# Optimization experiments

Measured on AMD Instinct MI355X. Metric: run time of the kernel, lower is better.

## Reference

```python
import jax, jax.numpy as jnp
import numpy as np

EPS = 1e-5
OFFSET_SCALE = 1.0
KPTS = 9   # 3x3 deformable kernel
GROUP = 1  # in_dim // out_dim


def _bn(x, g, b, m, v):
    # eval-mode BatchNorm2d on (B,C,H,W)
    s = g / jnp.sqrt(v + EPS)
    return x * s[None, :, None, None] + (b - m * s)[None, :, None, None]


def _dcnv4_core(value, offset, mask, offset_scale):
    # value: (B,H,W,G,Cg); offset: (B,H,W,G,K,2) as (dx,dy); mask: (B,H,W,G,K)
    B, H, W, G, Cg = value.shape
    K = mask.shape[-1]
    dt = value.dtype
    ky = jnp.repeat(jnp.arange(3) - 1, 3).astype(dt)
    kx = jnp.tile(jnp.arange(3) - 1, 3).astype(dt)
    grid = jnp.stack([kx, ky], -1)                                   # (K,2)
    base = jnp.stack(jnp.meshgrid(jnp.arange(W, dtype=dt),
                                  jnp.arange(H, dtype=dt),
                                  indexing='xy'), -1)                # (H,W,2) = (x,y)
    loc = base[None, :, :, None, None, :] + (grid + offset) * offset_scale  # (B,H,W,G,K,2)
    px, py = loc[..., 0], loc[..., 1]
    x0 = jnp.floor(px); y0 = jnp.floor(py)
    fx = px - x0; fy = py - y0
    vflat = value.transpose(0, 3, 1, 2, 4).reshape(B, G, H * W, Cg)
    out = jnp.zeros((B, G, H * W, Cg), dt)
    corners = ((0.0, 0.0, (1 - fx) * (1 - fy)), (1.0, 0.0, fx * (1 - fy)),
               (0.0, 1.0, (1 - fx) * fy), (1.0, 1.0, fx * fy))
    for dx, dy, wgt in corners:
        xi = x0 + dx; yi = y0 + dy
        valid = ((xi >= 0) & (xi < W) & (yi >= 0) & (yi < H)).astype(dt)
        idx = (jnp.clip(yi, 0, W and H - 1) * W + jnp.clip(xi, 0, W - 1)).astype(jnp.int32)
        idx = idx.transpose(0, 3, 1, 2, 4).reshape(B, G, H * W * K)
        v = jnp.take_along_axis(vflat, idx[..., None], axis=2).reshape(B, G, H * W, K, Cg)
        w = (wgt * valid * mask).transpose(0, 3, 1, 2, 4).reshape(B, G, H * W, K)
        out = out + jnp.einsum('bgsk,bgskc->bgsc', w, v)
    return out.reshape(B, G, H, W, Cg).transpose(0, 2, 3, 1, 4).reshape(B, H, W, G * Cg)


def setup_inputs() -> dict:
    key = jax.random.key(0)
    B, C, H, W = 8, 128, 64, 64
    C_OUT = 128
    OM = ((GROUP * KPTS * 3 + 7) // 8) * 8  # 32, offset_mask padded width
    ks = jax.random.split(key, 16)
    f = jnp.float32
    sc = 1.0 / np.sqrt(C).astype(np.float32)
    return {
        'x': jax.random.normal(ks[0], (B, C, H, W), f),
        'bn1_g': jax.random.uniform(ks[1], (C,), f, 0.5, 1.5),
        'bn1_b': jax.random.normal(ks[2], (C,), f) * 0.1,
        'bn1_m': jax.random.normal(ks[3], (C,), f) * 0.1,
        'bn1_v': jax.random.uniform(ks[4], (C,), f, 0.5, 1.5),
        'w_pw0': jax.random.normal(ks[5], (C, C), f) * sc,
        'w_vp': jax.random.normal(ks[6], (C, C), f) * sc,
        'b_vp': jnp.zeros((C,), f),
        'w_om': jax.random.normal(ks[7], (C, OM), f) * 0.01,
        'b_om': jnp.zeros((OM,), f),
        'w_op': jax.random.normal(ks[8], (C, C), f) * sc,
        'bn2_g': jax.random.uniform(ks[9], (C,), f, 0.5, 1.5),
        'bn2_b': jax.random.normal(ks[10], (C,), f) * 0.1,
        'bn2_m': jax.random.normal(ks[11], (C,), f) * 0.1,
        'bn2_v': jax.random.uniform(ks[12], (C,), f, 0.5, 1.5),
        'w_pw1': jax.random.normal(ks[13], (C_OUT, C), f) * sc,
    }


def reference(x, bn1_g, bn1_b, bn1_m, bn1_v, w_pw0, w_vp, b_vp, w_om, b_om, w_op,
              bn2_g, bn2_b, bn2_m, bn2_v, w_pw1):
    x = _bn(x, bn1_g, bn1_b, bn1_m, bn1_v)
    x = jnp.einsum('bchw,oc->bohw', x, w_pw0)
    B, C, H, W = x.shape
    x = x.reshape(B, H * W, C)  # raw reshape (faithful to torch .reshape, NOT a permute)
    G, K = GROUP, KPTS
    Cg = C // G
    value = (x @ w_vp + b_vp).reshape(B, H, W, G, Cg)
    om = (x @ w_om + b_om)[..., :G * K * 3].reshape(B, H, W, G, K, 3)
    out = _dcnv4_core(value, om[..., :2], om[..., 2], OFFSET_SCALE)
    out = out.reshape(B, H * W, C) @ w_op
    x = out.reshape(B, C, H, W)  # raw reshape back
    x = _bn(x, bn2_g, bn2_b, bn2_m, bn2_v)
    x = jnp.einsum('bchw,oc->bohw', x, w_pw1)
    return x
```

## Files before the change

### kernel.cpp

```cpp
#include <hip/hip_runtime.h>

#define HW 4096
#define PADF 33
#define PADU 136
typedef unsigned short ushort;
typedef __attribute__((ext_vector_type(8))) short short8;
typedef __attribute__((ext_vector_type(4))) float f32x4;

__device__ __forceinline__ ushort bf_rne(float f) {
  unsigned u = __float_as_uint(f);
  unsigned r = (u + 0x7fffu + ((u >> 16) & 1u)) >> 16;
  return (ushort)r;
}
__device__ __forceinline__ void split2(float f, ushort& hi, ushort& lo) {
  ushort h = bf_rne(f);
  float hf = __uint_as_float((unsigned)h << 16);
  hi = h;
  lo = bf_rne(f - hf);
}

__global__ __launch_bounds__(256) void prep(
    const float* __restrict__ g1, const float* __restrict__ be1,
    const float* __restrict__ m1, const float* __restrict__ v1,
    const float* __restrict__ w0,
    const float* __restrict__ g2, const float* __restrict__ be2,
    const float* __restrict__ m2, const float* __restrict__ v2,
    const float* __restrict__ w1,
    const float* __restrict__ wvp, const float* __restrict__ wom,
    const float* __restrict__ wop,
    ushort* __restrict__ W0h, ushort* __restrict__ W0l, float* __restrict__ b0,
    ushort* __restrict__ W1h, ushort* __restrict__ W1l, float* __restrict__ b1,
    ushort* __restrict__ vph, ushort* __restrict__ vpl,
    ushort* __restrict__ oph, ushort* __restrict__ opl,
    ushort* __restrict__ omh, ushort* __restrict__ oml)
{
  const int t = threadIdx.x;
  const int role = blockIdx.x;
  if (role < 16) {
    __shared__ float sc[128], sh[128], part[16][17];
    const int cv = role >> 3;
    const float* g  = cv ? g2 : g1;
    const float* be = cv ? be2 : be1;
    const float* mm = cv ? m2 : m1;
    const float* vv = cv ? v2 : v1;
    if (t < 128) {
      float s = g[t] / sqrtf(vv[t] + 1e-5f);
      sc[t] = s;
      sh[t] = be[t] - mm[t] * s;
    }
    __syncthreads();
    const float* ws = cv ? w1 : w0;
    ushort* dh = cv ? W1h : W0h;
    ushort* dl = cv ? W1l : W0l;
    float* bb  = cv ? b1 : b0;
    const int o = ((role & 7) << 4) + (t >> 4);
    const int kl = t & 15;
    float accb = 0.f;
    #pragma unroll
    for (int j = 0; j < 8; ++j) {
      const int k = (kl << 3) + j;
      const float wv = ws[o * 128 + k];
      ushort hi, lo;
      split2(wv * sc[k], hi, lo);
      dh[o * 128 + k] = hi;
      dl[o * 128 + k] = lo;
      accb = fmaf(wv, sh[k], accb);
    }
    part[t >> 4][kl] = accb;
    __syncthreads();
    if (kl == 0) {
      float s = 0.f;
      #pragma unroll
      for (int j = 0; j < 16; ++j) s += part[t >> 4][j];
      bb[o] = s;
    }
  } else if (role < 32) {
    const int rr = role & 7;
    const float* srcM = (role < 24) ? wvp : wop;
    ushort* dh = (role < 24) ? vph : oph;
    ushort* dl = (role < 24) ? vpl : opl;
    const int n = (rr << 4) + (t >> 4);
    const int kl = t & 15;
    #pragma unroll
    for (int j = 0; j < 8; ++j) {
      const int k = (kl << 3) + j;
      ushort hi, lo;
      split2(srcM[k * 128 + n], hi, lo);
      dh[n * 128 + k] = hi;
      dl[n * 128 + k] = lo;
    }
  } else {
    const int n = ((role - 32) << 4) + (t >> 4);
    const int kl = t & 15;
    #pragma unroll
    for (int j = 0; j < 8; ++j) {
      const int k = (kl << 3) + j;
      ushort hi, lo;
      split2(wom[k * 32 + n], hi, lo);
      omh[n * 128 + k] = hi;
      oml[n * 128 + k] = lo;
    }
  }
}

__global__ __launch_bounds__(512, 2) void fused_x_valom(
    const float* __restrict__ x,
    const ushort* __restrict__ W0h, const ushort* __restrict__ W0l,
    const float* __restrict__ b0,
    const ushort* __restrict__ vph, const ushort* __restrict__ vpl,
    const float* __restrict__ bvp, const float* __restrict__ bom,
    float* __restrict__ value, float* __restrict__ omb)
{
  __shared__ __align__(16) char smem[102912];
  __shared__ float b0_s[128], b2_s[160];
  ushort (*Wh_s)[32] = (ushort(*)[32])(smem);
  ushort (*Wl_s)[32] = (ushort(*)[32])(smem + 8192);
  float*  Xf         = (float*)(smem + 16384);
  ushort (*Vh_s)[32] = (ushort(*)[32])(smem);
  ushort (*Vl_s)[32] = (ushort(*)[32])(smem + 10240);
  ushort (*Yh)[PADU] = (ushort(*)[PADU])(smem + 33280);
  ushort (*Yl)[PADU] = (ushort(*)[PADU])(smem + 68096);

  const int t = threadIdx.x;
  const int cb = blockIdx.x;
  const int b = blockIdx.y;
  const int hwBase = cb << 7;
  const size_t xbase = (size_t)b * (size_t)(128 * HW);
  if (t < 128) b0_s[t] = b0[t];
  if (t < 160) b2_s[t] = (t < 128) ? bvp[t] : bom[t - 128];
  const int lane = t & 63, w = t >> 6;
  const int col = lane & 15, quad = lane >> 4;
  const f32x4 z = {0.f, 0.f, 0.f, 0.f};

  f32x4 acc1[8];
  #pragma unroll
  for (int f = 0; f < 8; ++f) acc1[f] = z;

  for (int kc = 0; kc < 4; ++kc) {
    const int kB = kc << 5;
    {
      const int o = t >> 2, q8 = (t & 3) << 3;
      *(uint4*)&Wh_s[o][q8] = *(const uint4*)&W0h[o * 128 + kB + q8];
      *(uint4*)&Wl_s[o][q8] = *(const uint4*)&W0l[o * 128 + kB + q8];
    }
    #pragma unroll
    for (int p = 0; p < 2; ++p) {
      const int idx = (p << 9) + t;
      const int c = idx >> 5, j4 = (idx & 31) << 2;
      const float4 f = *(const float4*)&x[xbase + (size_t)(kB + c) * HW + hwBase + j4];
      Xf[(j4 + 0) * PADF + c] = f.x;
      Xf[(j4 + 1) * PADF + c] = f.y;
      Xf[(j4 + 2) * PADF + c] = f.z;
      Xf[(j4 + 3) * PADF + c] = f.w;
    }
    __syncthreads();
    union { ushort u[8]; short8 v; } bh, bl;
    {
      const float* xr = &Xf[((w << 4) + col) * PADF + (quad << 3)];
      #pragma unroll
      for (int j = 0; j < 8; ++j) split2(xr[j], bh.u[j], bl.u[j]);
    }
    #pragma unroll
    for (int f = 0; f < 8; ++f) {
      const int row = (f << 4) + col;
      const short8 aH = *(const short8*)&Wh_s[row][quad << 3];
      const short8 aL = *(const short8*)&Wl_s[row][quad << 3];
      acc1[f] = __builtin_amdgcn_mfma_f32_16x16x32_bf16(aH, bh.v, acc1[f], 0, 0, 0);
      acc1[f] = __builtin_amdgcn_mfma_f32_16x16x32_bf16(aH, bl.v, acc1[f], 0, 0, 0);
      acc1[f] = __builtin_amdgcn_mfma_f32_16x16x32_bf16(aL, bh.v, acc1[f], 0, 0, 0);
    }
    __syncthreads();
  }

  #pragma unroll
  for (int f = 0; f < 8; ++f)
    #pragma unroll
    for (int r = 0; r < 4; ++r) {
      const int o = (f << 4) + (quad << 2) + r;
      const int j = (w << 4) + col;
      ushort hi, lo;
      split2(acc1[f][r] + b0_s[o], hi, lo);
      Yh[o][j] = hi;
      Yl[o][j] = lo;
    }

  const int wm2 = (w & 3) << 5;
  const int wn2 = (w >> 2) * 80;
  f32x4 acc2[2][5];
  #pragma unroll
  for (int i = 0; i < 2; ++i)
    #pragma unroll
    for (int j = 0; j < 5; ++j) acc2[i][j] = z;

  for (int j2 = 0; j2 < 4; ++j2) {
    for (int i = t; i < 640; i += 512) {
      const int n = i >> 2, q8 = (i & 3) << 3;
      *(uint4*)&Vh_s[n][q8] = *(const uint4*)&vph[n * 128 + (j2 << 5) + q8];
      *(uint4*)&Vl_s[n][q8] = *(const uint4*)&vpl[n * 128 + (j2 << 5) + q8];
    }
    __syncthreads();
    short8 aH[2], aL[2];
    #pragma unroll
    for (int f2 = 0; f2 < 2; ++f2) {
      const int row = wm2 + (f2 << 4) + col;
      aH[f2] = *(const short8*)&Yh[row][(j2 << 5) + (quad << 3)];
      aL[f2] = *(const short8*)&Yl[row][(j2 << 5) + (quad << 3)];
    }
    #pragma unroll
    for (int g2 = 0; g2 < 5; ++g2) {
      const int n = wn2 + (g2 << 4) + col;
      const short8 vh = *(const short8*)&Vh_s[n][quad << 3];
      const short8 vl = *(const short8*)&Vl_s[n][quad << 3];
      #pragma unroll
      for (int f2 = 0; f2 < 2; ++f2) {
        acc2[f2][g2] = __builtin_amdgcn_mfma_f32_16x16x32_bf16(aH[f2], vh, acc2[f2][g2], 0, 0, 0);
        acc2[f2][g2] = __builtin_amdgcn_mfma_f32_16x16x32_bf16(aH[f2], vl, acc2[f2][g2], 0, 0, 0);
        acc2[f2][g2] = __builtin_amdgcn_mfma_f32_16x16x32_bf16(aL[f2], vh, acc2[f2][g2], 0, 0, 0);
      }
    }
    __syncthreads();
  }
  #pragma unroll
  for (int f2 = 0; f2 < 2; ++f2)
    #pragma unroll
    for (int r = 0; r < 4; ++r) {
      const int m = wm2 + (f2 << 4) + (quad << 2) + r;
      const size_t gRow = (size_t)b * HW + (size_t)m * 32 + cb;
      #pragma unroll
      for (int g2 = 0; g2 < 5; ++g2) {
        const int n = wn2 + (g2 << 4) + col;
        const float v = acc2[f2][g2][r] + b2_s[n];
        if (n < 128) value[gRow * 128 + n] = v;
        else         omb[gRow * 32 + (n - 128)] = v;
      }
    }
}

__global__ __launch_bounds__(256) void dcn_sample(
    const float* __restrict__ value, const float* __restrict__ om,
    ushort* __restrict__ samph, ushort* __restrict__ sampl)
{
  __shared__ float oms[8][32];
  const int t = threadIdx.x;
  const int blk = blockIdx.x;
  const int b = blk & 7;
  const int sBase = (blk >> 3) << 3;
  const int s = sBase + (t >> 5);
  const int cg = (t & 31) << 2;
  oms[t >> 5][t & 31] = om[((size_t)b * HW + sBase + (t >> 5)) * 32 + (t & 31)];
  __syncthreads();
  const int h = s >> 6, wq = s & 63;
  const float* vb = value + (size_t)b * HW * 128;
  const float* omp = oms[t >> 5];
  const float fw = (float)wq, fh = (float)h;
  float4 acc = {0.f, 0.f, 0.f, 0.f};
  #pragma unroll
  for (int k = 0; k < 9; ++k) {
    const float kx = (float)(k % 3 - 1);
    const float ky = (float)(k / 3 - 1);
    const float dx = omp[k * 3 + 0];
    const float dy = omp[k * 3 + 1];
    const float m  = omp[k * 3 + 2];
    const float px = fw + kx + dx;
    const float py = fh + ky + dy;
    const float x0f = floorf(px), y0f = floorf(py);
    const float fx = px - x0f, fy = py - y0f;
    const int ix = (int)x0f, iy = (int)y0f;
    #pragma unroll
    for (int cy = 0; cy < 2; ++cy) {
      const int yi = iy + cy;
      const float wy = cy ? fy : 1.f - fy;
      const float vy = (yi >= 0 && yi < 64) ? 1.f : 0.f;
      const int yc = min(max(yi, 0), 63);
      #pragma unroll
      for (int cx = 0; cx < 2; ++cx) {
        const int xi = ix + cx;
        const float wx = cx ? fx : 1.f - fx;
        const float vx = (xi >= 0 && xi < 64) ? 1.f : 0.f;
        const int xc = min(max(xi, 0), 63);
        const float wgt = wx * wy * vx * vy * m;
        const float4 v = *(const float4*)&vb[(size_t)(yc * 64 + xc) * 128 + cg];
        acc.x = fmaf(wgt, v.x, acc.x);
        acc.y = fmaf(wgt, v.y, acc.y);
        acc.z = fmaf(wgt, v.z, acc.z);
        acc.w = fmaf(wgt, v.w, acc.w);
      }
    }
  }
  ushort h0, l0, h1, l1, h2, l2, h3, l3;
  split2(acc.x, h0, l0); split2(acc.y, h1, l1);
  split2(acc.z, h2, l2); split2(acc.w, h3, l3);
  const size_t idx = ((size_t)b * HW + s) * 128 + cg;
  uint2 uh, ul;
  uh.x = (unsigned)h0 | ((unsigned)h1 << 16);
  uh.y = (unsigned)h2 | ((unsigned)h3 << 16);
  ul.x = (unsigned)l0 | ((unsigned)l1 << 16);
  ul.y = (unsigned)l2 | ((unsigned)l3 << 16);
  *(uint2*)&samph[idx] = uh;
  *(uint2*)&sampl[idx] = ul;
}

__global__ __launch_bounds__(512, 2) void fused_op_out(
    const ushort* __restrict__ samph, const ushort* __restrict__ sampl,
    const ushort* __restrict__ oph, const ushort* __restrict__ opl,
    const ushort* __restrict__ W1h, const ushort* __restrict__ W1l,
    const float* __restrict__ b1, float* __restrict__ out)
{
  __shared__ __align__(16) char smem[102400];
  __shared__ float b1_s[128];
  ushort (*Ah_s)[32]  = (ushort(*)[32])(smem);
  ushort (*Al_s)[32]  = (ushort(*)[32])(smem + 8192);
  ushort (*Bh_s)[32]  = (ushort(*)[32])(smem + 16384);
  ushort (*Bl_s)[32]  = (ushort(*)[32])(smem + 24576);
  ushort (*W1h_s)[32] = (ushort(*)[32])(smem);
  ushort (*W1l_s)[32] = (ushort(*)[32])(smem + 8192);
  ushort (*Yh)[PADU]  = (ushort(*)[PADU])(smem + 32768);
  ushort (*Yl)[PADU]  = (ushort(*)[PADU])(smem + 67584);

  const int t = threadIdx.x;
  const int cb = blockIdx.x;
  const int b = blockIdx.y;
  if (t < 128) b1_s[t] = b1[t];
  const int lane = t & 63, w = t >> 6;
  const int col = lane & 15, quad = lane >> 4;
  const f32x4 z = {0.f, 0.f, 0.f, 0.f};

  const int wm1 = (w & 1) << 6, wn1 = (w >> 1) << 5;
  f32x4 acc1[4][2];
  #pragma unroll
  for (int i = 0; i < 4; ++i) { acc1[i][0] = z; acc1[i][1] = z; }

  for (int kc = 0; kc < 4; ++kc) {
    const int kB = kc << 5;
    {
      const int m = t >> 2, q8 = (t & 3) << 3;
      const size_t row = (size_t)b * HW + (size_t)m * 32 + cb;
      *(uint4*)&Ah_s[m][q8] = *(const uint4*)&samph[row * 128 + kB + q8];
      *(uint4*)&Al_s[m][q8] = *(const uint4*)&sampl[row * 128 + kB + q8];
      *(uint4*)&Bh_s[m][q8] = *(const uint4*)&oph[m * 128 + kB + q8];
      *(uint4*)&Bl_s[m][q8] = *(const uint4*)&opl[m * 128 + kB + q8];
    }
    __syncthreads();
    short8 aH[4], aL[4];
    #pragma unroll
    for (int f = 0; f < 4; ++f) {
      const int row = wm1 + (f << 4) + col;
      aH[f] = *(const short8*)&Ah_s[row][quad << 3];
      aL[f] = *(const short8*)&Al_s[row][quad << 3];
    }
    #pragma unroll
    for (int g = 0; g < 2; ++g) {
      const int n = wn1 + (g << 4) + col;
      const short8 bh = *(const short8*)&Bh_s[n][quad << 3];
      const short8 bl = *(const short8*)&Bl_s[n][quad << 3];
      #pragma unroll
      for (int f = 0; f < 4; ++f) {
        acc1[f][g] = __builtin_amdgcn_mfma_f32_16x16x32_bf16(aH[f], bh, acc1[f][g], 0, 0, 0);
        acc1[f][g] = __builtin_amdgcn_mfma_f32_16x16x32_bf16(aH[f], bl, acc1[f][g], 0, 0, 0);
        acc1[f][g] = __builtin_amdgcn_mfma_f32_16x16x32_bf16(aL[f], bh, acc1[f][g], 0, 0, 0);
      }
    }
    __syncthreads();
  }

  #pragma unroll
  for (int f = 0; f < 4; ++f)
    #pragma unroll
    for (int g = 0; g < 2; ++g)
      #pragma unroll
      for (int r = 0; r < 4; ++r) {
        const int ch = wm1 + (f << 4) + (quad << 2) + r;
        const int j  = wn1 + (g << 4) + col;
        ushort hi, lo;
        split2(acc1[f][g][r], hi, lo);
        Yh[j][ch] = hi;
        Yl[j][ch] = lo;
      }

  const int wm2 = (w & 1) << 6, wn2 = (w >> 1) << 5;
  f32x4 acc2[4][2];
  #pragma unroll
  for (int i = 0; i < 4; ++i) { acc2[i][0] = z; acc2[i][1] = z; }

  for (int j2 = 0; j2 < 4; ++j2) {
    {
      const int o = t >> 2, q8 = (t & 3) << 3;
      *(uint4*)&W1h_s[o][q8] = *(const uint4*)&W1h[o * 128 + (j2 << 5) + q8];
      *(uint4*)&W1l_s[o][q8] = *(const uint4*)&W1l[o * 128 + (j2 << 5) + q8];
    }
    __syncthreads();
    short8 aH[4], aL[4];
    #pragma unroll
    for (int f2 = 0; f2 < 4; ++f2) {
      const int row = wm2 + (f2 << 4) + col;
      aH[f2] = *(const short8*)&W1h_s[row][quad << 3];
      aL[f2] = *(const short8*)&W1l_s[row][quad << 3];
    }
    #pragma unroll
    for (int g2 = 0; g2 < 2; ++g2) {
      const int j = wn2 + (g2 << 4) + col;
      const short8 bh = *(const short8*)&Yh[j][(j2 << 5) + (quad << 3)];
      const short8 bl = *(const short8*)&Yl[j][(j2 << 5) + (quad << 3)];
      #pragma unroll
      for (int f2 = 0; f2 < 4; ++f2) {
        acc2[f2][g2] = __builtin_amdgcn_mfma_f32_16x16x32_bf16(aH[f2], bh, acc2[f2][g2], 0, 0, 0);
        acc2[f2][g2] = __builtin_amdgcn_mfma_f32_16x16x32_bf16(aH[f2], bl, acc2[f2][g2], 0, 0, 0);
        acc2[f2][g2] = __builtin_amdgcn_mfma_f32_16x16x32_bf16(aL[f2], bh, acc2[f2][g2], 0, 0, 0);
      }
    }
    __syncthreads();
  }
  const size_t obase = (size_t)b * (size_t)(128 * HW) + ((size_t)cb << 7);
  #pragma unroll
  for (int f2 = 0; f2 < 4; ++f2)
    #pragma unroll
    for (int r = 0; r < 4; ++r) {
      const int o = wm2 + (f2 << 4) + (quad << 2) + r;
      #pragma unroll
      for (int g2 = 0; g2 < 2; ++g2) {
        const int j = wn2 + (g2 << 4) + col;
        out[obase + (size_t)o * HW + j] = acc2[f2][g2][r] + b1_s[o];
      }
    }
}

extern "C" void kernel_launch(void* const* d_in, const int* in_sizes, int n_in,
                              void* d_out, int out_size, void* d_ws, size_t ws_size,
                              hipStream_t stream)
{
  const float* x    = (const float*)d_in[0];
  const float* g1   = (const float*)d_in[1];
  const float* be1  = (const float*)d_in[2];
  const float* m1   = (const float*)d_in[3];
  const float* v1   = (const float*)d_in[4];
  const float* wpw0 = (const float*)d_in[5];
  const float* wvp  = (const float*)d_in[6];
  const float* bvp  = (const float*)d_in[7];
  const float* womW = (const float*)d_in[8];
  const float* bom  = (const float*)d_in[9];
  const float* wop  = (const float*)d_in[10];
  const float* g2   = (const float*)d_in[11];
  const float* be2  = (const float*)d_in[12];
  const float* m2   = (const float*)d_in[13];
  const float* v2   = (const float*)d_in[14];
  const float* wpw1 = (const float*)d_in[15];

  char* ws = (char*)d_ws;
  float*  value = (float*) (ws + 0);
  float*  omb   = (float*) (ws + 16777216);
  ushort* samph = (ushort*)(ws + 20971520);
  ushort* sampl = (ushort*)(ws + 29360128);
  size_t o = 37748736;
  ushort* W0h = (ushort*)(ws + o); o += 32768;
  ushort* W0l = (ushort*)(ws + o); o += 32768;
  ushort* W1h = (ushort*)(ws + o); o += 32768;
  ushort* W1l = (ushort*)(ws + o); o += 32768;
  ushort* vph = (ushort*)(ws + o); o += 40960;
  ushort* vpl = (ushort*)(ws + o); o += 40960;
  ushort* oph = (ushort*)(ws + o); o += 32768;
  ushort* opl = (ushort*)(ws + o); o += 32768;
  float*  b0  = (float*)(ws + o);  o += 512;
  float*  b1  = (float*)(ws + o);
  ushort* omh = vph + 128 * 128;
  ushort* oml = vpl + 128 * 128;

  prep<<<34, 256, 0, stream>>>(g1, be1, m1, v1, wpw0, g2, be2, m2, v2, wpw1,
                               wvp, womW, wop,
                               W0h, W0l, b0, W1h, W1l, b1,
                               vph, vpl, oph, opl, omh, oml);
  fused_x_valom<<<dim3(32, 8), 512, 0, stream>>>(x, W0h, W0l, b0, vph, vpl,
                                                 bvp, bom, value, omb);
  dcn_sample<<<dim3(4096), 256, 0, stream>>>(value, omb, samph, sampl);
  fused_op_out<<<dim3(32, 8), 512, 0, stream>>>(samph, sampl, oph, opl,
                                                W1h, W1l, b1, (float*)d_out);
}
```

Before: 146.4 us.

## Fuse deformable sampling into op/out GEMM kernel and stage whole weights in LDS

Removes the separate dcn_sample kernel. Its bilinear sampling now runs inside the fused output kernel, which writes the bf16 hi/lo split straight to shared memory instead of round-tripping samph/sampl through global memory. Both fused GEMM kernels also load full weight matrices and input tiles into LDS once up front, replacing per-k-chunk loads, which drops most __syncthreads. LDS use rises to about 148-152KB per block, which likely limits occupancy to one block per CU. The fused kernel uses only 256 blocks where the sampling kernel had 4096, so the latency-bound gathers get less parallelism.

```diff
diff --git a/kernel.cpp b/kernel.cpp
--- a/kernel.cpp
+++ b/kernel.cpp
@@ -1,7 +1,6 @@
 #include <hip/hip_runtime.h>
 
 #define HW 4096
-#define PADF 33
 #define PADU 136
 typedef unsigned short ushort;
 typedef __attribute__((ext_vector_type(8))) short short8;
@@ -111,15 +110,15 @@
     const float* __restrict__ bvp, const float* __restrict__ bom,
     float* __restrict__ value, float* __restrict__ omb)
 {
-  __shared__ __align__(16) char smem[102912];
+  __shared__ __align__(16) char smem[151552];
   __shared__ float b0_s[128], b2_s[160];
-  ushort (*Wh_s)[32] = (ushort(*)[32])(smem);
-  ushort (*Wl_s)[32] = (ushort(*)[32])(smem + 8192);
-  float*  Xf         = (float*)(smem + 16384);
-  ushort (*Vh_s)[32] = (ushort(*)[32])(smem);
-  ushort (*Vl_s)[32] = (ushort(*)[32])(smem + 10240);
-  ushort (*Yh)[PADU] = (ushort(*)[PADU])(smem + 33280);
-  ushort (*Yl)[PADU] = (ushort(*)[PADU])(smem + 68096);
+  ushort (*Wh_s)[128][32] = (ushort(*)[128][32])(smem);
+  ushort (*Wl_s)[128][32] = (ushort(*)[128][32])(smem + 32768);
+  float  (*Xf)[128][33]   = (float(*)[128][33])(smem + 65536);
+  ushort (*Yh)[PADU]      = (ushort(*)[PADU])(smem);
+  ushort (*Yl)[PADU]      = (ushort(*)[PADU])(smem + 34816);
+  ushort (*Vh_s)[160][32] = (ushort(*)[160][32])(smem + 69632);
+  ushort (*Vl_s)[160][32] = (ushort(*)[160][32])(smem + 110592);
 
   const int t = threadIdx.x;
   const int cb = blockIdx.x;
@@ -132,46 +131,64 @@
   const int col = lane & 15, quad = lane >> 4;
   const f32x4 z = {0.f, 0.f, 0.f, 0.f};
 
+  {
+    const int o = t >> 2, q8 = (t & 3) << 3;
+    #pragma unroll
+    for (int kc = 0; kc < 4; ++kc) {
+      *(uint4*)&Wh_s[kc][o][q8] = *(const uint4*)&W0h[o * 128 + (kc << 5) + q8];
+      *(uint4*)&Wl_s[kc][o][q8] = *(const uint4*)&W0l[o * 128 + (kc << 5) + q8];
+    }
+  }
+  {
+    float4 xr4[8];
+    #pragma unroll
+    for (int i = 0; i < 8; ++i) {
+      const int idx8 = (i << 9) + t;
+      xr4[i] = *(const float4*)&x[xbase + (size_t)(idx8 >> 5) * HW + hwBase + ((idx8 & 31) << 2)];
+    }
+    #pragma unroll
+    for (int i = 0; i < 8; ++i) {
+      const int idx8 = (i << 9) + t;
+      const int ch = idx8 >> 5, j4 = (idx8 & 31) << 2;
+      Xf[ch >> 5][j4 + 0][ch & 31] = xr4[i].x;
+      Xf[ch >> 5][j4 + 1][ch & 31] = xr4[i].y;
+      Xf[ch >> 5][j4 + 2][ch & 31] = xr4[i].z;
+      Xf[ch >> 5][j4 + 3][ch & 31] = xr4[i].w;
+    }
+  }
+  __syncthreads();
+
   f32x4 acc1[8];
   #pragma unroll
   for (int f = 0; f < 8; ++f) acc1[f] = z;
 
+  #pragma unroll
   for (int kc = 0; kc < 4; ++kc) {
-    const int kB = kc << 5;
-    {
-      const int o = t >> 2, q8 = (t & 3) << 3;
-      *(uint4*)&Wh_s[o][q8] = *(const uint4*)&W0h[o * 128 + kB + q8];
-      *(uint4*)&Wl_s[o][q8] = *(const uint4*)&W0l[o * 128 + kB + q8];
-    }
-    #pragma unroll
-    for (int p = 0; p < 2; ++p) {
-      const int idx = (p << 9) + t;
-      const int c = idx >> 5, j4 = (idx & 31) << 2;
-      const float4 f = *(const float4*)&x[xbase + (size_t)(kB + c) * HW + hwBase + j4];
-      Xf[(j4 + 0) * PADF + c] = f.x;
-      Xf[(j4 + 1) * PADF + c] = f.y;
-      Xf[(j4 + 2) * PADF + c] = f.z;
-      Xf[(j4 + 3) * PADF + c] = f.w;
-    }
-    __syncthreads();
     union { ushort u[8]; short8 v; } bh, bl;
     {
-      const float* xr = &Xf[((w << 4) + col) * PADF + (quad << 3)];
+      const float* xr = Xf[kc][(w << 4) + col] + (quad << 3);
       #pragma unroll
       for (int j = 0; j < 8; ++j) split2(xr[j], bh.u[j], bl.u[j]);
     }
     #pragma unroll
     for (int f = 0; f < 8; ++f) {
       const int row = (f << 4) + col;
-      const short8 aH = *(const short8*)&Wh_s[row][quad << 3];
-      const short8 aL = *(const short8*)&Wl_s[row][quad << 3];
+      const short8 aH = *(const short8*)&Wh_s[kc][row][quad << 3];
+      const short8 aL = *(const short8*)&Wl_s[kc][row][quad << 3];
       acc1[f] = __builtin_amdgcn_mfma_f32_16x16x32_bf16(aH, bh.v, acc1[f], 0, 0, 0);
       acc1[f] = __builtin_amdgcn_mfma_f32_16x16x32_bf16(aH, bl.v, acc1[f], 0, 0, 0);
       acc1[f] = __builtin_amdgcn_mfma_f32_16x16x32_bf16(aL, bh.v, acc1[f], 0, 0, 0);
     }
-    __syncthreads();
-  }
-
+  }
+  __syncthreads();
+
+  for (int i = t; i < 2560; i += 512) {
+    const int kc = i / 640;
+    const int r2 = i - kc * 640;
+    const int n = r2 >> 2, q8 = (r2 & 3) << 3;
+    *(uint4*)&Vh_s[kc][n][q8] = *(const uint4*)&vph[n * 128 + (kc << 5) + q8];
+    *(uint4*)&Vl_s[kc][n][q8] = *(const uint4*)&vpl[n * 128 + (kc << 5) + q8];
+  }
   #pragma unroll
   for (int f = 0; f < 8; ++f)
     #pragma unroll
@@ -183,6 +200,7 @@
       Yh[o][j] = hi;
       Yl[o][j] = lo;
     }
+  __syncthreads();
 
   const int wm2 = (w & 3) << 5;
   const int wn2 = (w >> 2) * 80;
@@ -192,13 +210,8 @@
     #pragma unroll
     for (int j = 0; j < 5; ++j) acc2[i][j] = z;
 
+  #pragma unroll
   for (int j2 = 0; j2 < 4; ++j2) {
-    for (int i = t; i < 640; i += 512) {
-      const int n = i >> 2, q8 = (i & 3) << 3;
-      *(uint4*)&Vh_s[n][q8] = *(const uint4*)&vph[n * 128 + (j2 << 5) + q8];
-      *(uint4*)&Vl_s[n][q8] = *(const uint4*)&vpl[n * 128 + (j2 << 5) + q8];
-    }
-    __syncthreads();
     short8 aH[2], aL[2];
     #pragma unroll
     for (int f2 = 0; f2 < 2; ++f2) {
@@ -209,8 +222,8 @@
     #pragma unroll
     for (int g2 = 0; g2 < 5; ++g2) {
       const int n = wn2 + (g2 << 4) + col;
-      const short8 vh = *(const short8*)&Vh_s[n][quad << 3];
-      const short8 vl = *(const short8*)&Vl_s[n][quad << 3];
+      const short8 vh = *(const short8*)&Vh_s[j2][n][quad << 3];
+      const short8 vl = *(const short8*)&Vl_s[j2][n][quad << 3];
       #pragma unroll
       for (int f2 = 0; f2 < 2; ++f2) {
         acc2[f2][g2] = __builtin_amdgcn_mfma_f32_16x16x32_bf16(aH[f2], vh, acc2[f2][g2], 0, 0, 0);
@@ -218,7 +231,6 @@
         acc2[f2][g2] = __builtin_amdgcn_mfma_f32_16x16x32_bf16(aL[f2], vh, acc2[f2][g2], 0, 0, 0);
       }
     }
-    __syncthreads();
   }
   #pragma unroll
   for (int f2 = 0; f2 < 2; ++f2)
@@ -236,86 +248,23 @@
     }
 }
 
-__global__ __launch_bounds__(256) void dcn_sample(
-    const float* __restrict__ value, const float* __restrict__ om,
-    ushort* __restrict__ samph, ushort* __restrict__ sampl)
-{
-  __shared__ float oms[8][32];
-  const int t = threadIdx.x;
-  const int blk = blockIdx.x;
-  const int b = blk & 7;
-  const int sBase = (blk >> 3) << 3;
-  const int s = sBase + (t >> 5);
-  const int cg = (t & 31) << 2;
-  oms[t >> 5][t & 31] = om[((size_t)b * HW + sBase + (t >> 5)) * 32 + (t & 31)];
-  __syncthreads();
-  const int h = s >> 6, wq = s & 63;
-  const float* vb = value + (size_t)b * HW * 128;
-  const float* omp = oms[t >> 5];
-  const float fw = (float)wq, fh = (float)h;
-  float4 acc = {0.f, 0.f, 0.f, 0.f};
-  #pragma unroll
-  for (int k = 0; k < 9; ++k) {
-    const float kx = (float)(k % 3 - 1);
-    const float ky = (float)(k / 3 - 1);
-    const float dx = omp[k * 3 + 0];
-    const float dy = omp[k * 3 + 1];
-    const float m  = omp[k * 3 + 2];
-    const float px = fw + kx + dx;
-    const float py = fh + ky + dy;
-    const float x0f = floorf(px), y0f = floorf(py);
-    const float fx = px - x0f, fy = py - y0f;
-    const int ix = (int)x0f, iy = (int)y0f;
-    #pragma unroll
-    for (int cy = 0; cy < 2; ++cy) {
-      const int yi = iy + cy;
-      const float wy = cy ? fy : 1.f - fy;
-      const float vy = (yi >= 0 && yi < 64) ? 1.f : 0.f;
-      const int yc = min(max(yi, 0), 63);
-      #pragma unroll
-      for (int cx = 0; cx < 2; ++cx) {
-        const int xi = ix + cx;
-        const float wx = cx ? fx : 1.f - fx;
-        const float vx = (xi >= 0 && xi < 64) ? 1.f : 0.f;
-        const int xc = min(max(xi, 0), 63);
-        const float wgt = wx * wy * vx * vy * m;
-        const float4 v = *(const float4*)&vb[(size_t)(yc * 64 + xc) * 128 + cg];
-        acc.x = fmaf(wgt, v.x, acc.x);
-        acc.y = fmaf(wgt, v.y, acc.y);
-        acc.z = fmaf(wgt, v.z, acc.z);
-        acc.w = fmaf(wgt, v.w, acc.w);
-      }
-    }
-  }
-  ushort h0, l0, h1, l1, h2, l2, h3, l3;
-  split2(acc.x, h0, l0); split2(acc.y, h1, l1);
-  split2(acc.z, h2, l2); split2(acc.w, h3, l3);
-  const size_t idx = ((size_t)b * HW + s) * 128 + cg;
-  uint2 uh, ul;
-  uh.x = (unsigned)h0 | ((unsigned)h1 << 16);
-  uh.y = (unsigned)h2 | ((unsigned)h3 << 16);
-  ul.x = (unsigned)l0 | ((unsigned)l1 << 16);
-  ul.y = (unsigned)l2 | ((unsigned)l3 << 16);
-  *(uint2*)&samph[idx] = uh;
-  *(uint2*)&sampl[idx] = ul;
-}
-
-__global__ __launch_bounds__(512, 2) void fused_op_out(
-    const ushort* __restrict__ samph, const ushort* __restrict__ sampl,
+__global__ __launch_bounds__(512, 2) void fused_sample_op_out(
+    const float* __restrict__ value, const float* __restrict__ omb,
     const ushort* __restrict__ oph, const ushort* __restrict__ opl,
     const ushort* __restrict__ W1h, const ushort* __restrict__ W1l,
     const float* __restrict__ b1, float* __restrict__ out)
 {
-  __shared__ __align__(16) char smem[102400];
+  __shared__ __align__(16) char smem[147456];
   __shared__ float b1_s[128];
-  ushort (*Ah_s)[32]  = (ushort(*)[32])(smem);
-  ushort (*Al_s)[32]  = (ushort(*)[32])(smem + 8192);
-  ushort (*Bh_s)[32]  = (ushort(*)[32])(smem + 16384);
-  ushort (*Bl_s)[32]  = (ushort(*)[32])(smem + 24576);
-  ushort (*W1h_s)[32] = (ushort(*)[32])(smem);
-  ushort (*W1l_s)[32] = (ushort(*)[32])(smem + 8192);
-  ushort (*Yh)[PADU]  = (ushort(*)[PADU])(smem + 32768);
-  ushort (*Yl)[PADU]  = (ushort(*)[PADU])(smem + 67584);
+  ushort (*Afh)[128][32]  = (ushort(*)[128][32])(smem);
+  ushort (*Afl)[128][32]  = (ushort(*)[128][32])(smem + 32768);
+  ushort (*Bh)[128][32]   = (ushort(*)[128][32])(smem + 65536);
+  ushort (*Bl)[128][32]   = (ushort(*)[128][32])(smem + 98304);
+  float  (*oms)[32]       = (float(*)[32])(smem + 131072);
+  ushort (*Yh)[PADU]      = (ushort(*)[PADU])(smem);
+  ushort (*Yl)[PADU]      = (ushort(*)[PADU])(smem + 34816);
+  ushort (*W1h_)[128][32] = (ushort(*)[128][32])(smem + 69632);
+  ushort (*W1l_)[128][32] = (ushort(*)[128][32])(smem + 102400);
 
   const int t = threadIdx.x;
   const int cb = blockIdx.x;
@@ -325,34 +274,103 @@
   const int col = lane & 15, quad = lane >> 4;
   const f32x4 z = {0.f, 0.f, 0.f, 0.f};
 
+  {
+    const int m0 = t >> 2, j8 = (t & 3) << 3;
+    const size_t orow = ((size_t)b * HW + m0 * 32 + cb) * 32;
+    *(float4*)&oms[m0][j8]     = *(const float4*)&omb[orow + j8];
+    *(float4*)&oms[m0][j8 + 4] = *(const float4*)&omb[orow + j8 + 4];
+  }
+  #pragma unroll
+  for (int i = 0; i < 4; ++i) {
+    const int idx = (i << 9) + t;
+    const int kc = idx >> 9, n = (idx >> 2) & 127, q8 = (idx & 3) << 3;
+    *(uint4*)&Bh[kc][n][q8] = *(const uint4*)&oph[n * 128 + (kc << 5) + q8];
+    *(uint4*)&Bl[kc][n][q8] = *(const uint4*)&opl[n * 128 + (kc << 5) + q8];
+  }
+  __syncthreads();
+
+  {
+    const int m = t >> 2, q = t & 3;
+    const int s = m * 32 + cb;
+    const int hh = s >> 6, wq = s & 63;
+    const float* vb = value + (size_t)b * HW * 128 + (q << 5);
+    const float fw = (float)wq, fh = (float)hh;
+    const float* omp = oms[m];
+    float4 acc[8];
+    #pragma unroll
+    for (int cc = 0; cc < 8; ++cc) acc[cc] = make_float4(0.f, 0.f, 0.f, 0.f);
+    #pragma unroll
+    for (int k = 0; k < 9; ++k) {
+      const float kx = (float)(k % 3 - 1);
+      const float ky = (float)(k / 3 - 1);
+      const float dx = omp[k * 3 + 0];
+      const float dy = omp[k * 3 + 1];
+      const float mw = omp[k * 3 + 2];
+      const float px = fw + kx + dx;
+      const float py = fh + ky + dy;
+      const float x0f = floorf(px), y0f = floorf(py);
+      const float fx = px - x0f, fy = py - y0f;
+      const int ix = (int)x0f, iy = (int)y0f;
+      #pragma unroll
+      for (int cy = 0; cy < 2; ++cy) {
+        const int yi = iy + cy;
+        const float wy = cy ? fy : 1.f - fy;
+        const float vy = (yi >= 0 && yi < 64) ? 1.f : 0.f;
+        const int yc = min(max(yi, 0), 63);
+        #pragma unroll
+        for (int cx = 0; cx < 2; ++cx) {
+          const int xi = ix + cx;
+          const float wx = cx ? fx : 1.f - fx;
+          const float vx = (xi >= 0 && xi < 64) ? 1.f : 0.f;
+          const int xc = min(max(xi, 0), 63);
+          const float wgt = wx * wy * vx * vy * mw;
+          const float* vp = vb + (size_t)(yc * 64 + xc) * 128;
+          #pragma unroll
+          for (int cc = 0; cc < 8; ++cc) {
+            const float4 v = *(const float4*)&vp[cc << 2];
+            acc[cc].x = fmaf(wgt, v.x, acc[cc].x);
+            acc[cc].y = fmaf(wgt, v.y, acc[cc].y);
+            acc[cc].z = fmaf(wgt, v.z, acc[cc].z);
+            acc[cc].w = fmaf(wgt, v.w, acc[cc].w);
+          }
+        }
+      }
+    }
+    #pragma unroll
+    for (int cc = 0; cc < 8; ++cc) {
+      ushort h0, l0, h1, l1, h2, l2, h3, l3;
+      split2(acc[cc].x, h0, l0); split2(acc[cc].y, h1, l1);
+      split2(acc[cc].z, h2, l2); split2(acc[cc].w, h3, l3);
+      uint2 uh, ul;
+      uh.x = (unsigned)h0 | ((unsigned)h1 << 16);
+      uh.y = (unsigned)h2 | ((unsigned)h3 << 16);
+      ul.x = (unsigned)l0 | ((unsigned)l1 << 16);
+      ul.y = (unsigned)l2 | ((unsigned)l3 << 16);
+      *(uint2*)&Afh[q][m][cc << 2] = uh;
+      *(uint2*)&Afl[q][m][cc << 2] = ul;
+    }
+  }
+  __syncthreads();
+
   const int wm1 = (w & 1) << 6, wn1 = (w >> 1) << 5;
   f32x4 acc1[4][2];
   #pragma unroll
   for (int i = 0; i < 4; ++i) { acc1[i][0] = z; acc1[i][1] = z; }
 
+  #pragma unroll
   for (int kc = 0; kc < 4; ++kc) {
-    const int kB = kc << 5;
-    {
-      const int m = t >> 2, q8 = (t & 3) << 3;
-      const size_t row = (size_t)b * HW + (size_t)m * 32 + cb;
-      *(uint4*)&Ah_s[m][q8] = *(const uint4*)&samph[row * 128 + kB + q8];
-      *(uint4*)&Al_s[m][q8] = *(const uint4*)&sampl[row * 128 + kB + q8];
-      *(uint4*)&Bh_s[m][q8] = *(const uint4*)&oph[m * 128 + kB + q8];
-      *(uint4*)&Bl_s[m][q8] = *(const uint4*)&opl[m * 128 + kB + q8];
-    }
-    __syncthreads();
     short8 aH[4], aL[4];
     #pragma unroll
     for (int f = 0; f < 4; ++f) {
       const int row = wm1 + (f << 4) + col;
-      aH[f] = *(const short8*)&Ah_s[row][quad << 3];
-      aL[f] = *(const short8*)&Al_s[row][quad << 3];
+      aH[f] = *(const short8*)&Afh[kc][row][quad << 3];
+      aL[f] = *(const short8*)&Afl[kc][row][quad << 3];
     }
     #pragma unroll
     for (int g = 0; g < 2; ++g) {
       const int n = wn1 + (g << 4) + col;
-      const short8 bh = *(const short8*)&Bh_s[n][quad << 3];
-      const short8 bl = *(const short8*)&Bl_s[n][quad << 3];
+      const short8 bh = *(const short8*)&Bh[kc][n][quad << 3];
+      const short8 bl = *(const short8*)&Bl[kc][n][quad << 3];
       #pragma unroll
       for (int f = 0; f < 4; ++f) {
         acc1[f][g] = __builtin_amdgcn_mfma_f32_16x16x32_bf16(aH[f], bh, acc1[f][g], 0, 0, 0);
@@ -360,9 +378,16 @@
         acc1[f][g] = __builtin_amdgcn_mfma_f32_16x16x32_bf16(aL[f], bh, acc1[f][g], 0, 0, 0);
       }
     }
-    __syncthreads();
-  }
-
+  }
+  __syncthreads();
+
+  #pragma unroll
+  for (int i = 0; i < 4; ++i) {
+    const int idx = (i << 9) + t;
+    const int kc = idx >> 9, n = (idx >> 2) & 127, q8 = (idx & 3) << 3;
+    *(uint4*)&W1h_[kc][n][q8] = *(const uint4*)&W1h[n * 128 + (kc << 5) + q8];
+    *(uint4*)&W1l_[kc][n][q8] = *(const uint4*)&W1l[n * 128 + (kc << 5) + q8];
+  }
   #pragma unroll
   for (int f = 0; f < 4; ++f)
     #pragma unroll
@@ -376,25 +401,21 @@
         Yh[j][ch] = hi;
         Yl[j][ch] = lo;
       }
+  __syncthreads();
 
   const int wm2 = (w & 1) << 6, wn2 = (w >> 1) << 5;
   f32x4 acc2[4][2];
   #pragma unroll
   for (int i = 0; i < 4; ++i) { acc2[i][0] = z; acc2[i][1] = z; }
 
+  #pragma unroll
   for (int j2 = 0; j2 < 4; ++j2) {
-    {
-      const int o = t >> 2, q8 = (t & 3) << 3;
-      *(uint4*)&W1h_s[o][q8] = *(const uint4*)&W1h[o * 128 + (j2 << 5) + q8];
-      *(uint4*)&W1l_s[o][q8] = *(const uint4*)&W1l[o * 128 + (j2 << 5) + q8];
-    }
-    __syncthreads();
     short8 aH[4], aL[4];
     #pragma unroll
     for (int f2 = 0; f2 < 4; ++f2) {
       const int row = wm2 + (f2 << 4) + col;
-      aH[f2] = *(const short8*)&W1h_s[row][quad << 3];
-      aL[f2] = *(const short8*)&W1l_s[row][quad << 3];
+      aH[f2] = *(const short8*)&W1h_[j2][row][quad << 3];
+      aL[f2] = *(const short8*)&W1l_[j2][row][quad << 3];
     }
     #pragma unroll
     for (int g2 = 0; g2 < 2; ++g2) {
@@ -408,7 +429,6 @@
         acc2[f2][g2] = __builtin_amdgcn_mfma_f32_16x16x32_bf16(aL[f2], bh, acc2[f2][g2], 0, 0, 0);
       }
     }
-    __syncthreads();
   }
   const size_t obase = (size_t)b * (size_t)(128 * HW) + ((size_t)cb << 7);
   #pragma unroll
@@ -448,9 +468,7 @@
   char* ws = (char*)d_ws;
   float*  value = (float*) (ws + 0);
   float*  omb   = (float*) (ws + 16777216);
-  ushort* samph = (ushort*)(ws + 20971520);
-  ushort* sampl = (ushort*)(ws + 29360128);
-  size_t o = 37748736;
+  size_t o = 20971520;
   ushort* W0h = (ushort*)(ws + o); o += 32768;
   ushort* W0l = (ushort*)(ws + o); o += 32768;
   ushort* W1h = (ushort*)(ws + o); o += 32768;
@@ -470,7 +488,6 @@
                                vph, vpl, oph, opl, omh, oml);
   fused_x_valom<<<dim3(32, 8), 512, 0, stream>>>(x, W0h, W0l, b0, vph, vpl,
                                                  bvp, bom, value, omb);
-  dcn_sample<<<dim3(4096), 256, 0, stream>>>(value, omb, samph, sampl);
-  fused_op_out<<<dim3(32, 8), 512, 0, stream>>>(samph, sampl, oph, opl,
-                                                W1h, W1l, b1, (float*)d_out);
-}
+  fused_sample_op_out<<<dim3(32, 8), 512, 0, stream>>>(value, omb, oph, opl,
+                                                       W1h, W1l, b1, (float*)d_out);
+}
```

Result: slower. 216.8 us (+48.1%).
